# Performance work log

Hardware: AMD Instinct MI355X
Metric: run time of the kernel (lower is better)

## Reference

```python
import jax, jax.numpy as jnp
import numpy as np

TOKENS, D_IN = 8192, 1024
E, D_OUT = 8, 1024
H = 2 * D_OUT  # Expert hidden = 2 * num_outputs


def setup_inputs() -> dict:
    key = jax.random.key(0)
    ks = jax.random.split(key, 4)
    s_in = 1.0 / np.sqrt(D_IN)
    s_h = 1.0 / np.sqrt(H)
    return {
        "x": jax.random.normal(ks[0], (TOKENS, D_IN), dtype=jnp.float32),
        "W1": jax.random.normal(ks[1], (E, D_IN, H), dtype=jnp.float32) * s_in,
        "b1": jnp.zeros((E, H), dtype=jnp.float32),
        "W2": jax.random.normal(ks[2], (E, H, D_OUT), dtype=jnp.float32) * s_h,
        "b2": jnp.zeros((E, D_OUT), dtype=jnp.float32),
        "Wg": jax.random.normal(ks[3], (D_IN, E), dtype=jnp.float32) * s_in,
        "bg": jnp.zeros((E,), dtype=jnp.float32),
    }


def reference(x, W1, b1, W2, b2, Wg, bg):
    # Gating: softmax over experts. gates: [N, E]
    gates = jax.nn.softmax(x @ Wg + bg, axis=-1)
    # All experts run densely: batched GEMM over expert axis.
    h = jax.nn.relu(jnp.einsum('nd,edh->neh', x, W1) + b1)       # [N, E, H]
    expert_out = jnp.einsum('neh,ehf->nef', h, W2) + b2          # [N, E, D_OUT]
    # Gate-weighted sum over experts (fused stack*gate->sum).
    return jnp.einsum('nef,ne->nf', expert_out, gates)            # [N, D_OUT]
```

## Files before the change

kernel.cpp:

```cpp
#include <hip/hip_runtime.h>
#include <stdint.h>

#define TOKENS 8192
#define D_IN   1024
#define NEXP   8
#define D_OUT  1024
#define HDIM   2048

typedef __bf16 bf16x8 __attribute__((ext_vector_type(8)));
typedef __bf16 bf16x4 __attribute__((ext_vector_type(4)));
typedef float  f32x4  __attribute__((ext_vector_type(4)));

__device__ __forceinline__ void gload16(const void* g, void* l) {
  __builtin_amdgcn_global_load_lds(
      (const __attribute__((address_space(1))) void*)g,
      (__attribute__((address_space(3))) void*)l,
      16, 0, 0);
}

template <int N>
__device__ __forceinline__ void waitv() {
  if constexpr (N == 0)      asm volatile("s_waitcnt vmcnt(0)" ::: "memory");
  else if constexpr (N == 1) asm volatile("s_waitcnt vmcnt(1)" ::: "memory");
  else if constexpr (N == 2) asm volatile("s_waitcnt vmcnt(2)" ::: "memory");
  else if constexpr (N == 3) asm volatile("s_waitcnt vmcnt(3)" ::: "memory");
  else if constexpr (N == 4) asm volatile("s_waitcnt vmcnt(4)" ::: "memory");
  else if constexpr (N == 5) asm volatile("s_waitcnt vmcnt(5)" ::: "memory");
  else if constexpr (N == 6) asm volatile("s_waitcnt vmcnt(6)" ::: "memory");
  else static_assert(N <= 6, "unsupported vmcnt");
}

__global__ void gate_cvt_kernel(const float* __restrict__ x,
                                const float* __restrict__ Wg,
                                const float* __restrict__ bg,
                                float* __restrict__ gates,
                                __bf16* __restrict__ xb) {
  const int lane = threadIdx.x & 63;
  const int n = blockIdx.x * 4 + (threadIdx.x >> 6);
  float acc[NEXP];
#pragma unroll
  for (int e = 0; e < NEXP; ++e) acc[e] = 0.f;
  const float* xr = x + (size_t)n * D_IN;
  __bf16* xo = xb + (size_t)n * D_IN;
#pragma unroll 4
  for (int d0 = 0; d0 < D_IN; d0 += 64) {
    const int d = d0 + lane;
    float xv = xr[d];
    xo[d] = (__bf16)xv;
    const float* wr = Wg + d * NEXP;
#pragma unroll
    for (int e = 0; e < NEXP; ++e) acc[e] += xv * wr[e];
  }
#pragma unroll
  for (int e = 0; e < NEXP; ++e) {
    float v = acc[e];
#pragma unroll
    for (int off = 32; off > 0; off >>= 1) v += __shfl_down(v, off);
    acc[e] = v;
  }
  if (lane == 0) {
    float mx = -1e30f;
#pragma unroll
    for (int e = 0; e < NEXP; ++e) { acc[e] += bg[e]; mx = fmaxf(mx, acc[e]); }
    float s = 0.f;
#pragma unroll
    for (int e = 0; e < NEXP; ++e) { acc[e] = expf(acc[e] - mx); s += acc[e]; }
    float inv = 1.f / s;
#pragma unroll
    for (int e = 0; e < NEXP; ++e) gates[n * NEXP + e] = acc[e] * inv;
  }
}

__global__ void transpose_cvt_kernel(const float* __restrict__ W,
                                     __bf16* __restrict__ Wt,
                                     int K, int N, int EPG) {
  __shared__ float tile[32][33];
  const int e = blockIdx.z;
  const int ldo = EPG * K;
  const float* Win = W + (size_t)e * K * N;
  __bf16* Wout = Wt + (size_t)(e / EPG) * N * ldo + (size_t)(e % EPG) * K;
  const int n0 = blockIdx.x * 32;
  const int k0 = blockIdx.y * 32;
  const int tx = threadIdx.x & 31;
  const int ty = threadIdx.x >> 5;
#pragma unroll
  for (int r = ty; r < 32; r += 8)
    tile[r][tx] = Win[(size_t)(k0 + r) * N + n0 + tx];
  __syncthreads();
#pragma unroll
  for (int r = ty; r < 32; r += 8)
    Wout[(size_t)(n0 + r) * ldo + k0 + tx] = (__bf16)tile[tx][r];
}

__global__ void merge_kernel(float* __restrict__ out,
                             const float* __restrict__ acc1,
                             const float* __restrict__ gates,
                             const float* __restrict__ b2,
                             int use_acc1) {
  const int idx = blockIdx.x * 256 + threadIdx.x;
  const int n = idx >> 8;
  const int fb = idx & 255;
  float4 o = ((const float4*)out)[idx];
  if (use_acc1) {
    float4 a = ((const float4*)acc1)[idx];
    o.x += a.x; o.y += a.y; o.z += a.z; o.w += a.w;
  }
  const float* g = gates + (size_t)n * NEXP;
#pragma unroll
  for (int e = 0; e < NEXP; ++e) {
    const float ge = g[e];
    float4 b = ((const float4*)(b2 + (size_t)e * D_OUT))[fb];
    o.x += ge * b.x; o.y += ge * b.y; o.z += ge * b.z; o.w += ge * b.w;
  }
  ((float4*)out)[idx] = o;
}

template <int NT, int BM, int BN, int WM, int WN, int EPI, int DBUF>
__global__ __launch_bounds__(NT, 2)
void moe_gemm(const __bf16* __restrict__ A, size_t AZ,
              const __bf16* __restrict__ B, size_t BZ,
              const float* __restrict__ b1g,
              const float* __restrict__ gates,
              int e0,
              __bf16* __restrict__ Hout, size_t HZ, int OCZ, int ldo,
              float* __restrict__ F0, float* __restrict__ F1,
              int first, int M, int N, int K) {
  constexpr int RM = BM / WM, RN = BN / WN;
  constexpr int FM = RM / 16, FN = RN / 16;
  constexpr int HM = FM / 2,  HN = FN / 2;
  constexpr int LA = BM * 4 / NT;
  constexpr int LB = BN * 4 / NT;
  constexpr int AELEM = BM * 64;
  constexpr int SLOT  = (BM + BN) * 64;
  static_assert(HM * HN * 2 == 16, "want 16-MFMA clusters");
  __shared__ alignas(16) __bf16 lds[DBUF * SLOT];

  const int tid  = threadIdx.x;
  const int lane = tid & 63;
  const int wave = tid >> 6;
  const int wr   = wave / WN;
  const int wc   = wave % WN;
  const int lrow = lane & 15;
  const int khi  = lane >> 4;
  const int sx   = (lrow & 7) << 3;
  const int bz   = blockIdx.z;

  A += (size_t)bz * AZ;
  B += (size_t)bz * BZ;

  const int Gx   = gridDim.x;
  const int nwg  = Gx * gridDim.y;
  const int orig = blockIdx.y * Gx + blockIdx.x;
  const int wgid = (orig & 7) * (nwg >> 3) + (orig >> 3);
  const int bn0  = (wgid % Gx) * BN;
  const int bm0  = (wgid / Gx) * BM;

  const __bf16* srcA[2][LA];
  const __bf16* srcB[2][LB];
#pragma unroll
  for (int q = 0; q < 2; ++q) {
#pragma unroll
    for (int j = 0; j < LA; ++j) {
      int o   = q * (BM * 64) + j * (NT * 16) + tid * 16;
      int row = o >> 7;
      int cb  = (o & 127) ^ ((row & 7) << 4);
      srcA[q][j] = A + (size_t)(bm0 + row) * K + (cb >> 1);
    }
#pragma unroll
    for (int j = 0; j < LB; ++j) {
      int o   = q * (BN * 64) + j * (NT * 16) + tid * 16;
      int row = o >> 7;
      int cb  = (o & 127) ^ ((row & 7) << 4);
      srcB[q][j] = B + (size_t)(bn0 + row) * K + (cb >> 1);
    }
  }

  auto stageA = [&](int kt, int q, int s) {
#pragma unroll
    for (int j = 0; j < LA; ++j)
      gload16(srcA[q][j] + (size_t)kt * 64,
              lds + s * SLOT + q * (BM * 32) + j * (NT * 8) + wave * 512);
  };
  auto stageB = [&](int kt, int q, int s) {
#pragma unroll
    for (int j = 0; j < LB; ++j)
      gload16(srcB[q][j] + (size_t)kt * 64,
              lds + s * SLOT + AELEM + q * (BN * 32) + j * (NT * 8) + wave * 512);
  };

  f32x4 acc[FM][FN];
#pragma unroll
  for (int m = 0; m < FM; ++m)
#pragma unroll
    for (int n = 0; n < FN; ++n) acc[m][n] = f32x4{0.f, 0.f, 0.f, 0.f};

  bf16x8 af[HM][2];
  bf16x8 bf[2][HN][2];

  auto rdA = [&](const __bf16* As, int mq) {
#pragma unroll
    for (int mi = 0; mi < HM; ++mi)
#pragma unroll
      for (int kk = 0; kk < 2; ++kk)
        af[mi][kk] = *(const bf16x8*)
            &As[(size_t)(mq * (BM / 2) + wr * (RM / 2) + mi * 16 + lrow) * 64 +
                ((kk * 32 + khi * 8) ^ sx)];
  };
  auto rdB = [&](const __bf16* Bs, int nq) {
#pragma unroll
    for (int ni = 0; ni < HN; ++ni)
#pragma unroll
      for (int kk = 0; kk < 2; ++kk)
        bf[nq][ni][kk] = *(const bf16x8*)
            &Bs[(size_t)(nq * (BN / 2) + wc * (RN / 2) + ni * 16 + lrow) * 64 +
                ((kk * 32 + khi * 8) ^ sx)];
  };
  auto cluster = [&](int mq, int nq) {
    __builtin_amdgcn_s_setprio(1);
#pragma unroll
    for (int kk = 0; kk < 2; ++kk)
#pragma unroll
      for (int mi = 0; mi < HM; ++mi)
#pragma unroll
        for (int ni = 0; ni < HN; ++ni)
          acc[mq * HM + mi][nq * HN + ni] =
              __builtin_amdgcn_mfma_f32_16x16x32_bf16(
                  af[mi][kk], bf[nq][ni][kk], acc[mq * HM + mi][nq * HN + ni],
                  0, 0, 0);
    __builtin_amdgcn_s_setprio(0);
  };

#define BAR()   asm volatile("s_barrier" ::: "memory")
#define LGKM0() do { asm volatile("s_waitcnt lgkmcnt(0)" ::: "memory"); \
                     __builtin_amdgcn_sched_barrier(0); } while (0)

  const int nk = K >> 6;

  if constexpr (DBUF == 1) {
    stageA(0, 0, 0); stageB(0, 0, 0); stageB(0, 1, 0);
    waitv<LB>();
    BAR();
    for (int t = 0; t < nk; ++t) {
      const bool pf = (t + 1 < nk);
      rdA(lds, 0); rdB(lds + AELEM, 0);
      stageA(t, 1, 0);
      BAR(); LGKM0();
      cluster(0, 0);
      waitv<LA>();
      BAR();
      rdB(lds + AELEM, 1);
      if (pf) stageA(t + 1, 0, 0);
      BAR(); LGKM0();
      cluster(0, 1);
      if (pf) waitv<LA>(); else waitv<0>();
      BAR();
      rdA(lds, 1);
      if (pf) stageB(t + 1, 0, 0);
      BAR(); LGKM0();
      cluster(1, 0);
      BAR();
      if (pf) stageB(t + 1, 1, 0);
      BAR();
      cluster(1, 1);
      if (pf) waitv<LB>();
      BAR();
    }
  } else {
    stageA(0, 0, 0); stageB(0, 0, 0); stageB(0, 1, 0); stageA(0, 1, 0);
    waitv<LA + LB>();
    BAR();
    for (int t = 0; t < nk; ++t) {
      const int s = t & 1;
      const __bf16* As = lds + s * SLOT;
      const __bf16* Bs = As + AELEM;
      const bool pf = (t + 1 < nk);
      rdA(As, 0); rdB(Bs, 0);
      if (pf) stageA(t + 1, 0, s ^ 1);
      BAR(); LGKM0();
      cluster(0, 0);
      if (pf) waitv<2 * LA>(); else waitv<LA>();
      BAR();
      rdB(Bs, 1);
      if (pf) stageB(t + 1, 0, s ^ 1);
      BAR(); LGKM0();
      cluster(0, 1);
      if (pf) waitv<LA + LB>(); else waitv<0>();
      BAR();
      rdA(As, 1);
      if (pf) stageB(t + 1, 1, s ^ 1);
      BAR(); LGKM0();
      cluster(1, 0);
      BAR();
      if (pf) stageA(t + 1, 1, s ^ 1);
      BAR();
      cluster(1, 1);
      if (pf) waitv<LA + LB>();
      BAR();
    }
  }

#undef BAR
#undef LGKM0

  const float* bias = (EPI == 0) ? b1g + (size_t)(e0 + bz) * HDIM : nullptr;
  const int ecol = e0 + bz;
  __bf16* Hp = (EPI == 0) ? Hout + (size_t)bz * HZ + (size_t)bz * OCZ : nullptr;
  float* F = (EPI == 3) ? (bz ? F1 : F0) : nullptr;

#pragma unroll
  for (int m = 0; m < FM; ++m) {
    const int grow0 = bm0 + (m / HM) * (BM / 2) + wr * (RM / 2) +
                      (m % HM) * 16 + khi * 4;
    if constexpr (EPI == 0) {
      float g[4];
#pragma unroll
      for (int r = 0; r < 4; ++r)
        g[r] = gates[(size_t)(grow0 + r) * NEXP + ecol];
#pragma unroll
      for (int n = 0; n < FN; ++n) {
        const int gcol = bn0 + (n / HN) * (BN / 2) + wc * (RN / 2) +
                         (n % HN) * 16 + lrow;
        const float bv = bias[gcol];
        f32x4 a = acc[m][n];
#pragma unroll
        for (int r = 0; r < 4; ++r) {
          float v = a[r] + bv;
          v = v > 0.f ? v : 0.f;
          Hp[(size_t)(grow0 + r) * ldo + gcol] = (__bf16)(v * g[r]);
        }
      }
    } else {
#pragma unroll
      for (int n = 0; n < FN; ++n) {
        const int gcol = bn0 + (n / HN) * (BN / 2) + wc * (RN / 2) +
                         (n % HN) * 16 + lrow;
        f32x4 a = acc[m][n];
#pragma unroll
        for (int r = 0; r < 4; ++r) {
          float* o = F + (size_t)(grow0 + r) * N + gcol;
          if (first) *o = a[r];
          else       *o += a[r];
        }
      }
    }
  }
}

extern "C" void kernel_launch(void* const* d_in, const int* in_sizes, int n_in,
                              void* d_out, int out_size, void* d_ws, size_t ws_size,
                              hipStream_t stream) {
  const float* x  = (const float*)d_in[0];
  const float* W1 = (const float*)d_in[1];
  const float* b1 = (const float*)d_in[2];
  const float* W2 = (const float*)d_in[3];
  const float* b2 = (const float*)d_in[4];
  const float* Wg = (const float*)d_in[5];
  const float* bg = (const float*)d_in[6];
  float* out = (float*)d_out;

  char* w = (char*)d_ws;
  float* gates = (float*)w;   w += (size_t)TOKENS * NEXP * 4;
  __bf16* xb   = (__bf16*)w;  w += (size_t)TOKENS * D_IN * 2;
  __bf16* w1t  = (__bf16*)w;  w += (size_t)NEXP * HDIM * D_IN * 2;
  __bf16* w2c  = (__bf16*)w;  w += (size_t)NEXP * D_OUT * HDIM * 2;
  const size_t base = (size_t)(w - (char*)d_ws);

  const size_t acc_b = (size_t)TOKENS * D_OUT * 4;
  const size_t h1_b  = (size_t)TOKENS * HDIM * 2;
  const int G = (ws_size >= base + acc_b + 4 * h1_b) ? 4
              : (ws_size >= base + acc_b + 2 * h1_b) ? 2 : 1;

  float* acc1 = nullptr;
  if (G > 1) { acc1 = (float*)w; w += acc_b; }
  __bf16* hbuf = (__bf16*)w;

  const size_t WSLICE = (size_t)HDIM * D_IN;

  gate_cvt_kernel<<<TOKENS / 4, 256, 0, stream>>>(x, Wg, bg, gates, xb);
  transpose_cvt_kernel<<<dim3(HDIM / 32, D_IN / 32, NEXP), 256, 0, stream>>>(
      W1, w1t, D_IN, HDIM, 1);
  transpose_cvt_kernel<<<dim3(D_OUT / 32, HDIM / 32, NEXP), 256, 0, stream>>>(
      W2, w2c, HDIM, D_OUT, (G == 4) ? 2 : 1);

  if (G == 4) {
    for (int d = 0; d < 2; ++d) {
      for (int i2 = 0; i2 < 2; ++i2) {
        const int e0 = 4 * d + 2 * i2;
        moe_gemm<512, 256, 256, 2, 4, 0, 1><<<dim3(8, 32, 2), 512, 0, stream>>>(
            xb, 0, w1t + (size_t)e0 * WSLICE, WSLICE, b1, gates, e0,
            hbuf + (size_t)i2 * TOKENS * 4096, 0, HDIM, 2 * HDIM,
            nullptr, nullptr, 0, TOKENS, HDIM, D_IN);
      }
      moe_gemm<512, 256, 256, 2, 4, 3, 2><<<dim3(4, 32, 2), 512, 0, stream>>>(
          hbuf, (size_t)TOKENS * 4096,
          w2c + (size_t)(2 * d) * D_OUT * 4096, (size_t)D_OUT * 4096,
          nullptr, nullptr, 0, nullptr, 0, 0, 0,
          out, acc1, (d == 0) ? 1 : 0, TOKENS, D_OUT, 2 * HDIM);
    }
  } else if (G == 2) {
    for (int d = 0; d < 4; ++d) {
      const int e0 = 2 * d;
      moe_gemm<512, 256, 256, 2, 4, 0, 1><<<dim3(8, 32, 2), 512, 0, stream>>>(
          xb, 0, w1t + (size_t)e0 * WSLICE, WSLICE, b1, gates, e0,
          hbuf, (size_t)TOKENS * HDIM, 0, HDIM,
          nullptr, nullptr, 0, TOKENS, HDIM, D_IN);
      moe_gemm<512, 256, 256, 2, 4, 3, 2><<<dim3(4, 32, 2), 512, 0, stream>>>(
          hbuf, (size_t)TOKENS * HDIM,
          w2c + (size_t)e0 * D_OUT * HDIM, (size_t)D_OUT * HDIM,
          nullptr, nullptr, 0, nullptr, 0, 0, 0,
          out, acc1, (d == 0) ? 1 : 0, TOKENS, D_OUT, HDIM);
    }
  } else {
    for (int e = 0; e < NEXP; ++e) {
      moe_gemm<512, 256, 256, 2, 4, 0, 1><<<dim3(8, 32, 1), 512, 0, stream>>>(
          xb, 0, w1t + (size_t)e * WSLICE, 0, b1, gates, e,
          hbuf, 0, 0, HDIM,
          nullptr, nullptr, 0, TOKENS, HDIM, D_IN);
      moe_gemm<512, 256, 256, 2, 4, 3, 2><<<dim3(4, 32, 1), 512, 0, stream>>>(
          hbuf, 0, w2c + (size_t)e * D_OUT * HDIM, 0,
          nullptr, nullptr, 0, nullptr, 0, 0, 0,
          out, nullptr, (e == 0) ? 1 : 0, TOKENS, D_OUT, HDIM);
    }
  }

  merge_kernel<<<TOKENS, 256, 0, stream>>>(out, acc1, gates, b2, (G > 1) ? 1 : 0);
}
```

Measured before the change: 659.2 us.

## Merge double-buffered GEMM main loop into two half-tile phases per K step

The double-buffered path of the MoE GEMM main loop now runs two phases per K step instead of four quadrant phases. Each phase reads a full half of the fragments and issues 32 MFMAs through a new cluster_h lambda, with both halves of the next stage's loads issued per phase. This halves the barriers and waitcnt points per iteration and gives larger MFMA bursts to hide global-to-LDS loads. In exchange it holds all B fragments in registers at once, which raises register pressure, and it changes the vmcnt wait accounting, which could expose load latency if the counts are off.

```diff
diff --git a/kernel.cpp b/kernel.cpp
--- a/kernel.cpp
+++ b/kernel.cpp
@@ -132,7 +132,7 @@
   constexpr int LB = BN * 4 / NT;
   constexpr int AELEM = BM * 64;
   constexpr int SLOT  = (BM + BN) * 64;
-  static_assert(HM * HN * 2 == 16, "want 16-MFMA clusters");
+  static_assert(HM * HN * 2 == 16, "want 16-MFMA quadrant clusters");
   __shared__ alignas(16) __bf16 lds[DBUF * SLOT];
 
   const int tid  = threadIdx.x;
@@ -227,6 +227,22 @@
               __builtin_amdgcn_mfma_f32_16x16x32_bf16(
                   af[mi][kk], bf[nq][ni][kk], acc[mq * HM + mi][nq * HN + ni],
                   0, 0, 0);
+    __builtin_amdgcn_s_setprio(0);
+  };
+  auto cluster_h = [&](int mq) {
+    __builtin_amdgcn_s_setprio(1);
+#pragma unroll
+    for (int kk = 0; kk < 2; ++kk)
+#pragma unroll
+      for (int mi = 0; mi < HM; ++mi)
+#pragma unroll
+        for (int nq = 0; nq < 2; ++nq)
+#pragma unroll
+          for (int ni = 0; ni < HN; ++ni)
+            acc[mq * HM + mi][nq * HN + ni] =
+                __builtin_amdgcn_mfma_f32_16x16x32_bf16(
+                    af[mi][kk], bf[nq][ni][kk], acc[mq * HM + mi][nq * HN + ni],
+                    0, 0, 0);
     __builtin_amdgcn_s_setprio(0);
   };
 
@@ -267,34 +283,24 @@
     }
   } else {
     stageA(0, 0, 0); stageB(0, 0, 0); stageB(0, 1, 0); stageA(0, 1, 0);
-    waitv<LA + LB>();
+    waitv<LA>();
     BAR();
     for (int t = 0; t < nk; ++t) {
       const int s = t & 1;
       const __bf16* As = lds + s * SLOT;
       const __bf16* Bs = As + AELEM;
       const bool pf = (t + 1 < nk);
-      rdA(As, 0); rdB(Bs, 0);
-      if (pf) stageA(t + 1, 0, s ^ 1);
+      rdA(As, 0); rdB(Bs, 0); rdB(Bs, 1);
+      if (pf) { stageA(t + 1, 0, s ^ 1); stageB(t + 1, 0, s ^ 1); }
       BAR(); LGKM0();
-      cluster(0, 0);
-      if (pf) waitv<2 * LA>(); else waitv<LA>();
-      BAR();
-      rdB(Bs, 1);
-      if (pf) stageB(t + 1, 0, s ^ 1);
+      cluster_h(0);
+      if (pf) waitv<LA + LB>(); else waitv<0>();
+      BAR();
+      rdA(As, 1);
+      if (pf) { stageB(t + 1, 1, s ^ 1); stageA(t + 1, 1, s ^ 1); }
       BAR(); LGKM0();
-      cluster(0, 1);
-      if (pf) waitv<LA + LB>(); else waitv<0>();
-      BAR();
-      rdA(As, 1);
-      if (pf) stageB(t + 1, 1, s ^ 1);
-      BAR(); LGKM0();
-      cluster(1, 0);
-      BAR();
-      if (pf) stageA(t + 1, 1, s ^ 1);
-      BAR();
-      cluster(1, 1);
-      if (pf) waitv<LA + LB>();
+      cluster_h(1);
+      if (pf) waitv<LA>();
       BAR();
     }
   }
```

Measured after the change: 669.5 us. Within noise of the previous version (+1.6%).
